# Kernel tuning notes

Measured on AMD Instinct MI355X. Metric: run time of the kernel, lower is better.

Reference implementation:

```python
import jax, jax.numpy as jnp
import numpy as np

INPUT_DIM = 256
DEPTH = 8
HIDDEN = 64
NUM_INNER = 2 ** DEPTH - 1   # 255
NUM_LEAVES = 2 ** DEPTH      # 256
BATCH = 8192


def _xavier(key, shape, fan_in, fan_out):
    bound = jnp.sqrt(6.0 / (fan_in + fan_out)).astype(jnp.float32)
    return jax.random.uniform(key, shape, jnp.float32, -bound, bound)


def setup_inputs() -> dict:
    key = jax.random.key(0)
    k = jax.random.split(key, 5)
    x = jax.random.normal(k[0], (BATCH, INPUT_DIM), jnp.float32)
    # Batched per-node MLP params (one slice per inner node)
    w1 = _xavier(k[1], (NUM_INNER, HIDDEN, INPUT_DIM), INPUT_DIM, HIDDEN)
    b1 = jnp.zeros((NUM_INNER, HIDDEN), jnp.float32)
    w2 = _xavier(k[2], (NUM_INNER, HIDDEN), HIDDEN, 1)
    b2 = jnp.zeros((NUM_INNER,), jnp.float32)
    leaf = _xavier(k[3], (NUM_LEAVES, 1), NUM_LEAVES, 1)
    return {"x": x, "w1": w1, "b1": b1, "w2": w2, "b2": b2, "leaf": leaf}


def reference(x, w1, b1, w2, b2, leaf):
    B = x.shape[0]
    # Fused per-node MLPs: hidden [B, N, H]
    h = jax.nn.relu(jnp.einsum("bi,nhi->bnh", x, w1) + b1)
    logits = jnp.einsum("bnh,nh->bn", h, w2) + b2        # [B, N]
    node_outputs = jax.nn.sigmoid(logits)                 # p, in BFS node order

    # Tree traversal: level-by-level interleave. Child of node j at a level
    # are 2j (left, weight 1-p) and 2j+1 (right, weight p) at the next level.
    reach_levels = []
    cur = jnp.ones((B, 1), x.dtype)
    for level in range(DEPTH):
        reach_levels.append(cur)
        lo = (1 << level) - 1
        p_lvl = node_outputs[:, lo : lo + (1 << level)]   # [B, 2^level]
        cur = jnp.stack([cur * (1.0 - p_lvl), cur * p_lvl], axis=-1).reshape(B, -1)
    node_reach = jnp.concatenate(reach_levels, axis=1)    # [B, NUM_INNER], BFS order
    path_probs = cur                                      # [B, NUM_LEAVES]

    h_out = (path_probs @ leaf)[:, 0]                     # [B]
    return h_out, path_probs, node_outputs, node_reach
```

## Files before the change

kernel.cpp:

```cpp
#include <hip/hip_runtime.h>
#include <cstdint>

#define BATCH   8192
#define KDIM    256
#define HID     64
#define NODES   255
#define NPG     16

typedef unsigned short u16;
typedef unsigned int u32;
typedef short bf16x8 __attribute__((ext_vector_type(8)));
typedef float f32x16 __attribute__((ext_vector_type(16)));


__device__ __forceinline__ u32 f2bf(float f) {
  u32 u = __float_as_uint(f);
  return (u + 0x7FFFu + ((u >> 16) & 1u)) >> 16;
}

__device__ __forceinline__ void gld_lds16(const void* g, void* l) {
  typedef __attribute__((address_space(1))) void* gp_t;
  typedef __attribute__((address_space(3))) void* lp_t;
  gp_t gp = reinterpret_cast<gp_t>(reinterpret_cast<uintptr_t>(g));
  lp_t lp = reinterpret_cast<lp_t>(static_cast<u32>(reinterpret_cast<uintptr_t>(l)));
  __builtin_amdgcn_global_load_lds(gp, lp, 16, 0, 0);
}


#define NPRM 16320

__global__ __launch_bounds__(256) void cvt_kernel(
    const float* __restrict__ x, const float* __restrict__ w1,
    const float* __restrict__ b1, const float* __restrict__ w2,
    u16* __restrict__ xpack, u16* __restrict__ w1pk,
    float* __restrict__ b1p, float* __restrict__ w2p) {
  const int tid = threadIdx.x;
  const int blk = blockIdx.x;

  if (blk < 256) {
    __shared__ u16 sT[32 * 268];
    const float* xs = x + (size_t)blk * 32 * KDIM;
#pragma unroll
    for (int j = 0; j < 8; ++j) {
      int idx = j * 256 + tid;
      float4 v = ((const float4*)xs)[idx];
      int row = idx >> 6, f4 = idx & 63;
      *(u32*)&sT[row * 268 + f4 * 4]     = f2bf(v.x) | (f2bf(v.y) << 16);
      *(u32*)&sT[row * 268 + f4 * 4 + 2] = f2bf(v.z) | (f2bf(v.w) << 16);
    }
    __syncthreads();
#pragma unroll
    for (int j = 0; j < 4; ++j) {
      int d = j * 256 + tid;
      int ks = d >> 6, hl = (d >> 5) & 1, l31 = d & 31;
      const u16* s8 = &sT[l31 * 268 + ks * 16 + hl * 8];
      u32 a = *(const u32*)s8, b = *(const u32*)(s8 + 2);
      u32 c = *(const u32*)(s8 + 4), e = *(const u32*)(s8 + 6);
      uint4 o = {a, b, c, e};
      ((uint4*)xpack)[(size_t)blk * 1024 + d] = o;
    }
  } else if (blk < 511) {
    __shared__ u16 sT[64 * 260];
    const int node = blk - 256;
    const float* src = w1 + (size_t)node * (HID * KDIM);
#pragma unroll
    for (int r = 0; r < 16; ++r) {
      int idx = r * 256 + tid;
      float4 v = ((const float4*)src)[idx];
      int h = idx >> 6, f4 = idx & 63;
      uint2 o;
      o.x = f2bf(v.x) | (f2bf(v.y) << 16);
      o.y = f2bf(v.z) | (f2bf(v.w) << 16);
      *(uint2*)&sT[h * 260 + f4 * 4] = o;
    }
    __syncthreads();
    u16* dst = w1pk + (size_t)node * (HID * KDIM);
#pragma unroll
    for (int r = 0; r < 8; ++r) {
      int g = r * 256 + tid;
      int kb = g >> 6, h = g & 63;
      const u16* s8 = &sT[h * 260 + kb * 8];
      uint2 lo = *(const uint2*)s8;
      uint2 hi = *(const uint2*)(s8 + 4);
      uint4 o = {lo.x, lo.y, hi.x, hi.y};
      ((uint4*)dst)[g] = o;
    }
  } else {
    int i2 = (blk - 511) * 256 + tid;
    if (i2 < 2 * NPRM) {
      int a = i2 >= NPRM;
      int j = a ? i2 - NPRM : i2;
      int reg = j & 15, rt = (j >> 4) & 1, hl = (j >> 5) & 1, node = j >> 6;
      int h = rt * 32 + (reg & 3) + 8 * (reg >> 2) + 4 * hl;
      float v = (a ? b1 : w2)[node * 64 + h];
      (a ? b1p : w2p)[j] = v;
    }
  }
}


__global__ __launch_bounds__(256, 2) void fused_mlp_kernel(
    const u16* __restrict__ xpack,
    const u16* __restrict__ w1pk,
    const float* __restrict__ b1p,
    const float* __restrict__ w2p,
    const float* __restrict__ b2,
    float* __restrict__ no_t)
{
  __shared__ __align__(16) u16 sW[2][16384];
  __shared__ __align__(16) float sW2[NPG * 64];
  __shared__ __align__(16) float sB1[NPG * 64];

  const int tid  = threadIdx.x;
  const int lane = tid & 63;
  const int wv   = tid >> 6;
  const int l31  = lane & 31;
  const int hl   = lane >> 5;
  const int nbase = blockIdx.y * NPG;

  auto stage_node = [&](int nodeIdx, int bufIdx) {
    const u16* base = w1pk + (size_t)nodeIdx * (HID * KDIM);
    char* lb = (char*)(&sW[bufIdx][0]);
#pragma unroll
    for (int j = 0; j < 8; ++j) {
      int s = j * 256 + tid;
      gld_lds16(base + s * 8, lb + s * 16);
    }
  };

  stage_node(nbase, 0);
  gld_lds16(w2p + (size_t)nbase * 64 + tid * 4, (char*)sW2 + tid * 16);
  gld_lds16(b1p + (size_t)nbase * 64 + tid * 4, (char*)sB1 + tid * 16);

  const int ctile0 = blockIdx.x * 8 + wv * 2;
  bf16x8 xf[2][16];
#pragma unroll
  for (int ct = 0; ct < 2; ++ct) {
    const u16* src = xpack + ((size_t)(ctile0 + ct) * 16) * 512 + lane * 8;
#pragma unroll
    for (int ks = 0; ks < 16; ++ks)
      xf[ct][ks] = *(const bf16x8*)(src + ks * 512);
  }

  const u32 abase = (u32)(hl * 64 + l31) * 16u;

  __syncthreads();
  int buf = 0;

  for (int i = 0; i < NPG; ++i) {
    const int node = nbase + i;

    if (i + 1 < NPG) stage_node(nbase + i + 1, buf ^ 1);

    f32x16 acc00, acc01, acc10, acc11;
    {
      const int o0 = i * 64 + hl * 32;
#pragma unroll
      for (int qd = 0; qd < 4; ++qd) {
        float4 b0 = *(const float4*)&sB1[o0 + qd * 4];
        float4 b1q = *(const float4*)&sB1[o0 + 16 + qd * 4];
#pragma unroll
        for (int e = 0; e < 4; ++e) {
          acc00[qd * 4 + e] = (&b0.x)[e];
          acc01[qd * 4 + e] = (&b0.x)[e];
          acc10[qd * 4 + e] = (&b1q.x)[e];
          acc11[qd * 4 + e] = (&b1q.x)[e];
        }
      }
    }

    const char* sw = (const char*)&sW[buf][0] + abase;
    __builtin_amdgcn_s_setprio(1);
#pragma unroll
    for (int ks = 0; ks < 16; ++ks) {
      bf16x8 a0 = *(const bf16x8*)(sw + ks * 2048);
      bf16x8 a1 = *(const bf16x8*)(sw + ks * 2048 + 512);
      acc00 = __builtin_amdgcn_mfma_f32_32x32x16_bf16(a0, xf[0][ks], acc00, 0, 0, 0);
      acc01 = __builtin_amdgcn_mfma_f32_32x32x16_bf16(a0, xf[1][ks], acc01, 0, 0, 0);
      acc10 = __builtin_amdgcn_mfma_f32_32x32x16_bf16(a1, xf[0][ks], acc10, 0, 0, 0);
      acc11 = __builtin_amdgcn_mfma_f32_32x32x16_bf16(a1, xf[1][ks], acc11, 0, 0, 0);
    }
    __builtin_amdgcn_s_setprio(0);

    float p0 = 0.f, p1 = 0.f;
#pragma unroll
    for (int qd = 0; qd < 4; ++qd) {
      int o = i * 64 + hl * 32 + qd * 4;
      float4 w0 = *(const float4*)&sW2[o];
      float4 w1q = *(const float4*)&sW2[o + 16];
#pragma unroll
      for (int e = 0; e < 4; ++e) {
        int r = qd * 4 + e;
        float w0e = (&w0.x)[e];
        float w1e = (&w1q.x)[e];
        p0 += fmaxf(acc00[r], 0.f) * w0e;
        p1 += fmaxf(acc01[r], 0.f) * w0e;
        p0 += fmaxf(acc10[r], 0.f) * w1e;
        p1 += fmaxf(acc11[r], 0.f) * w1e;
      }
    }
    p0 += __shfl_xor(p0, 32);
    p1 += __shfl_xor(p1, 32);

    if (node < NODES) {
      float pv = hl ? p1 : p0;
      float sig = 1.0f / (1.0f + expf(-(pv + b2[node])));
      no_t[(size_t)node * BATCH + blockIdx.x * 256 + wv * 64 + lane] = sig;
    }

    asm volatile("s_waitcnt vmcnt(1)" ::: "memory");
    __builtin_amdgcn_s_barrier();
    __builtin_amdgcn_sched_barrier(0);

    buf ^= 1;
  }
}


__global__ __launch_bounds__(256) void tree_kernel(
    const float* __restrict__ no_t,
    const float* __restrict__ leaf,
    float* __restrict__ out)
{
  __shared__ float p[16][257];

  const int tid = threadIdx.x;
  const int bbase = blockIdx.x * 16;
  const int wave = tid >> 6;
  const int lane = tid & 63;

  for (int i = tid; i < NODES * 16; i += 256) {
    int n = i >> 4, r = i & 15;
    p[r][n] = no_t[(size_t)n * BATCH + bbase + r];
  }
  __syncthreads();

  float4 lw = ((const float4*)leaf)[lane];

  float* h_out  = out;
  float* pp_out = out + 8192;
  float* no_out = out + 8192 + 8192 * 256;
  float* nr_out = out + 8192 + 8192 * 256 + 8192 * (size_t)NODES;

  for (int j = 0; j < 4; ++j) {
    const int r = wave * 4 + j;
    const int b = bbase + r;
    const float* pr = p[r];
    float* nr_b = nr_out + (size_t)b * NODES;

    float rc = 1.f;
#pragma unroll
    for (int L = 0; L < 6; ++L) {
      if (lane < (1 << L)) nr_b[(1 << L) - 1 + lane] = rc;
      float par = __shfl(rc, lane >> 1);
      float pv = pr[(1 << L) - 1 + (lane >> 1)];
      rc = par * ((lane & 1) ? pv : (1.f - pv));
    }
    nr_b[63 + lane] = rc;
    float p6 = pr[63 + lane];
    float r7a = rc * (1.f - p6), r7b = rc * p6;
    nr_b[127 + 2 * lane]     = r7a;
    nr_b[127 + 2 * lane + 1] = r7b;
    float p7a = pr[127 + 2 * lane], p7b = pr[127 + 2 * lane + 1];
    float4 pp;
    pp.x = r7a * (1.f - p7a);
    pp.y = r7a * p7a;
    pp.z = r7b * (1.f - p7b);
    pp.w = r7b * p7b;
    ((float4*)(pp_out + (size_t)b * 256))[lane] = pp;

    float* no_b = no_out + (size_t)b * NODES;
#pragma unroll
    for (int k = 0; k < 4; ++k) {
      int n = lane + 64 * k;
      if (n < NODES) no_b[n] = pr[n];
    }

    float hacc = pp.x * lw.x + pp.y * lw.y + pp.z * lw.z + pp.w * lw.w;
    hacc += __shfl_xor(hacc, 1);
    hacc += __shfl_xor(hacc, 2);
    hacc += __shfl_xor(hacc, 4);
    hacc += __shfl_xor(hacc, 8);
    hacc += __shfl_xor(hacc, 16);
    hacc += __shfl_xor(hacc, 32);
    if (lane == 0) h_out[b] = hacc;
  }
}


extern "C" void kernel_launch(void* const* d_in, const int* in_sizes, int n_in,
                              void* d_out, int out_size, void* d_ws, size_t ws_size,
                              hipStream_t stream) {
  const float* x    = (const float*)d_in[0];
  const float* w1   = (const float*)d_in[1];
  const float* b1   = (const float*)d_in[2];
  const float* w2   = (const float*)d_in[3];
  const float* b2   = (const float*)d_in[4];
  const float* leaf = (const float*)d_in[5];
  float* out = (float*)d_out;

  char* ws = (char*)d_ws;
  u16*   xpack = (u16*)ws;
  u16*   w1pk  = (u16*)(ws + (size_t)4194304);
  float* w2p   = (float*)(ws + (size_t)12582912);
  float* b1p   = (float*)(ws + (size_t)12648192);
  float* no_t  = (float*)(ws + (size_t)12713472);

  cvt_kernel<<<639, 256, 0, stream>>>(x, w1, b1, w2, xpack, w1pk, b1p, w2p);

  dim3 g(32, 16);
  fused_mlp_kernel<<<g, 256, 0, stream>>>(xpack, w1pk, b1p, w2p, b2, no_t);

  tree_kernel<<<BATCH / 16, 256, 0, stream>>>(no_t, leaf, out);
}
```

Before: 153.9 us.

## Split K into halves, stream x from global, and shrink node groups for occupancy

Nodes per block drop from 16 to 4, so the grid grows to 32x64 blocks. W1 staging is split into two K-halves in a 2x8192 LDS buffer. Only half of the x fragments stay in registers, and the other half is reloaded from global memory between the two half-MFMA passes. The goal is to cut registers and LDS so that three blocks fit per CU, and to spread work over more blocks. In exchange, x is re-read from global/L2 for every node, and each node now needs extra barriers.

```diff
diff --git a/kernel.cpp b/kernel.cpp
--- a/kernel.cpp
+++ b/kernel.cpp
@@ -5,7 +5,7 @@
 #define KDIM    256
 #define HID     64
 #define NODES   255
-#define NPG     16
+#define NPG     4
 
 typedef unsigned short u16;
 typedef unsigned int u32;
@@ -99,7 +99,7 @@
 }
 
 
-__global__ __launch_bounds__(256, 2) void fused_mlp_kernel(
+__global__ __launch_bounds__(256, 3) void fused_mlp_kernel(
     const u16* __restrict__ xpack,
     const u16* __restrict__ w1pk,
     const float* __restrict__ b1p,
@@ -107,7 +107,7 @@
     const float* __restrict__ b2,
     float* __restrict__ no_t)
 {
-  __shared__ __align__(16) u16 sW[2][16384];
+  __shared__ __align__(16) u16 sW[2][8192];
   __shared__ __align__(16) float sW2[NPG * 64];
   __shared__ __align__(16) float sB1[NPG * 64];
 
@@ -118,46 +118,50 @@
   const int hl   = lane >> 5;
   const int nbase = blockIdx.y * NPG;
 
-  auto stage_node = [&](int nodeIdx, int bufIdx) {
-    const u16* base = w1pk + (size_t)nodeIdx * (HID * KDIM);
+  auto stage_half = [&](int iLocal, int half, int bufIdx) {
+    const u16* base = w1pk + (size_t)(nbase + iLocal) * 16384 + half * 8192;
     char* lb = (char*)(&sW[bufIdx][0]);
 #pragma unroll
-    for (int j = 0; j < 8; ++j) {
+    for (int j = 0; j < 4; ++j) {
       int s = j * 256 + tid;
       gld_lds16(base + s * 8, lb + s * 16);
     }
   };
 
-  stage_node(nbase, 0);
-  gld_lds16(w2p + (size_t)nbase * 64 + tid * 4, (char*)sW2 + tid * 16);
-  gld_lds16(b1p + (size_t)nbase * 64 + tid * 4, (char*)sB1 + tid * 16);
+  stage_half(0, 0, 0);
+  if (tid < 64) {
+    gld_lds16(w2p + (size_t)nbase * 64 + tid * 4, (char*)sW2 + tid * 16);
+  } else if (tid < 128) {
+    int t = tid - 64;
+    gld_lds16(b1p + (size_t)nbase * 64 + t * 4, (char*)sB1 + t * 16);
+  }
 
   const int ctile0 = blockIdx.x * 8 + wv * 2;
-  bf16x8 xf[2][16];
-#pragma unroll
-  for (int ct = 0; ct < 2; ++ct) {
-    const u16* src = xpack + ((size_t)(ctile0 + ct) * 16) * 512 + lane * 8;
-#pragma unroll
-    for (int ks = 0; ks < 16; ++ks)
-      xf[ct][ks] = *(const bf16x8*)(src + ks * 512);
+  const u16* xs0 = xpack + (size_t)(ctile0 + 0) * 8192 + lane * 8;
+  const u16* xs1 = xpack + (size_t)(ctile0 + 1) * 8192 + lane * 8;
+  bf16x8 xf0[8], xf1[8];
+#pragma unroll
+  for (int ks = 0; ks < 8; ++ks) {
+    xf0[ks] = *(const bf16x8*)(xs0 + ks * 512);
+    xf1[ks] = *(const bf16x8*)(xs1 + ks * 512);
   }
 
   const u32 abase = (u32)(hl * 64 + l31) * 16u;
 
   __syncthreads();
-  int buf = 0;
 
   for (int i = 0; i < NPG; ++i) {
-    const int node = nbase + i;
-
-    if (i + 1 < NPG) stage_node(nbase + i + 1, buf ^ 1);
+    const int fc = i & 1;
+    const int oc = fc ^ 1;
+
+    stage_half(i, oc, 1);
 
     f32x16 acc00, acc01, acc10, acc11;
     {
       const int o0 = i * 64 + hl * 32;
 #pragma unroll
       for (int qd = 0; qd < 4; ++qd) {
-        float4 b0 = *(const float4*)&sB1[o0 + qd * 4];
+        float4 b0  = *(const float4*)&sB1[o0 + qd * 4];
         float4 b1q = *(const float4*)&sB1[o0 + 16 + qd * 4];
 #pragma unroll
         for (int e = 0; e < 4; ++e) {
@@ -169,50 +173,65 @@
       }
     }
 
-    const char* sw = (const char*)&sW[buf][0] + abase;
-    __builtin_amdgcn_s_setprio(1);
-#pragma unroll
-    for (int ks = 0; ks < 16; ++ks) {
-      bf16x8 a0 = *(const bf16x8*)(sw + ks * 2048);
-      bf16x8 a1 = *(const bf16x8*)(sw + ks * 2048 + 512);
-      acc00 = __builtin_amdgcn_mfma_f32_32x32x16_bf16(a0, xf[0][ks], acc00, 0, 0, 0);
-      acc01 = __builtin_amdgcn_mfma_f32_32x32x16_bf16(a0, xf[1][ks], acc01, 0, 0, 0);
-      acc10 = __builtin_amdgcn_mfma_f32_32x32x16_bf16(a1, xf[0][ks], acc10, 0, 0, 0);
-      acc11 = __builtin_amdgcn_mfma_f32_32x32x16_bf16(a1, xf[1][ks], acc11, 0, 0, 0);
-    }
-    __builtin_amdgcn_s_setprio(0);
+    {
+      const char* sw = (const char*)&sW[0][0] + abase;
+      const u16* nx0 = xs0 + oc * 4096;
+      const u16* nx1 = xs1 + oc * 4096;
+#pragma unroll
+      for (int ks = 0; ks < 8; ++ks) {
+        bf16x8 a0 = *(const bf16x8*)(sw + ks * 2048);
+        bf16x8 a1 = *(const bf16x8*)(sw + ks * 2048 + 512);
+        acc00 = __builtin_amdgcn_mfma_f32_32x32x16_bf16(a0, xf0[ks], acc00, 0, 0, 0);
+        acc01 = __builtin_amdgcn_mfma_f32_32x32x16_bf16(a0, xf1[ks], acc01, 0, 0, 0);
+        acc10 = __builtin_amdgcn_mfma_f32_32x32x16_bf16(a1, xf0[ks], acc10, 0, 0, 0);
+        acc11 = __builtin_amdgcn_mfma_f32_32x32x16_bf16(a1, xf1[ks], acc11, 0, 0, 0);
+        xf0[ks] = *(const bf16x8*)(nx0 + ks * 512);
+        xf1[ks] = *(const bf16x8*)(nx1 + ks * 512);
+      }
+    }
+    __syncthreads();
+
+    if (i + 1 < NPG) stage_half(i + 1, oc, 0);
+
+    {
+      const char* sw = (const char*)&sW[1][0] + abase;
+#pragma unroll
+      for (int ks = 0; ks < 8; ++ks) {
+        bf16x8 a0 = *(const bf16x8*)(sw + ks * 2048);
+        bf16x8 a1 = *(const bf16x8*)(sw + ks * 2048 + 512);
+        acc00 = __builtin_amdgcn_mfma_f32_32x32x16_bf16(a0, xf0[ks], acc00, 0, 0, 0);
+        acc01 = __builtin_amdgcn_mfma_f32_32x32x16_bf16(a0, xf1[ks], acc01, 0, 0, 0);
+        acc10 = __builtin_amdgcn_mfma_f32_32x32x16_bf16(a1, xf0[ks], acc10, 0, 0, 0);
+        acc11 = __builtin_amdgcn_mfma_f32_32x32x16_bf16(a1, xf1[ks], acc11, 0, 0, 0);
+      }
+    }
 
     float p0 = 0.f, p1 = 0.f;
 #pragma unroll
     for (int qd = 0; qd < 4; ++qd) {
       int o = i * 64 + hl * 32 + qd * 4;
-      float4 w0 = *(const float4*)&sW2[o];
+      float4 w0  = *(const float4*)&sW2[o];
       float4 w1q = *(const float4*)&sW2[o + 16];
 #pragma unroll
       for (int e = 0; e < 4; ++e) {
         int r = qd * 4 + e;
-        float w0e = (&w0.x)[e];
-        float w1e = (&w1q.x)[e];
-        p0 += fmaxf(acc00[r], 0.f) * w0e;
-        p1 += fmaxf(acc01[r], 0.f) * w0e;
-        p0 += fmaxf(acc10[r], 0.f) * w1e;
-        p1 += fmaxf(acc11[r], 0.f) * w1e;
+        p0 += fmaxf(acc00[r], 0.f) * (&w0.x)[e];
+        p1 += fmaxf(acc01[r], 0.f) * (&w0.x)[e];
+        p0 += fmaxf(acc10[r], 0.f) * (&w1q.x)[e];
+        p1 += fmaxf(acc11[r], 0.f) * (&w1q.x)[e];
       }
     }
     p0 += __shfl_xor(p0, 32);
     p1 += __shfl_xor(p1, 32);
 
+    const int node = nbase + i;
     if (node < NODES) {
       float pv = hl ? p1 : p0;
       float sig = 1.0f / (1.0f + expf(-(pv + b2[node])));
       no_t[(size_t)node * BATCH + blockIdx.x * 256 + wv * 64 + lane] = sig;
     }
 
-    asm volatile("s_waitcnt vmcnt(1)" ::: "memory");
-    __builtin_amdgcn_s_barrier();
-    __builtin_amdgcn_sched_barrier(0);
-
-    buf ^= 1;
+    if (i + 1 < NPG) __syncthreads();
   }
 }
 
@@ -308,7 +327,7 @@
 
   cvt_kernel<<<639, 256, 0, stream>>>(x, w1, b1, w2, xpack, w1pk, b1p, w2p);
 
-  dim3 g(32, 16);
+  dim3 g(32, 64);
   fused_mlp_kernel<<<g, 256, 0, stream>>>(xpack, w1pk, b1p, w2p, b2, no_t);
 
   tree_kernel<<<BATCH / 16, 256, 0, stream>>>(no_t, leaf, out);
```

Result: slower. 162.2 us (+5.4%).

## Merge three kernels into one cooperative persistent kernel with grid syncs

Applied to the files above, without the earlier changes.

Replaces the separate convert, fused-MLP and tree kernels with a single cooperative launch that loops over the old block indices and uses grid-wide syncs between phases. Shared memory is a union so each phase reuses the same allocation. The aim is to remove the launch gaps and tail effects between kernels. In exchange it adds grid.sync overhead and hipOccupancy queries on the host. It also replaces the per-node vmcnt-based wait with a full __syncthreads, which may weaken the overlap between staging and MFMA.

```diff
diff --git a/kernel.cpp b/kernel.cpp
--- a/kernel.cpp
+++ b/kernel.cpp
@@ -1,11 +1,15 @@
 #include <hip/hip_runtime.h>
+#include <hip/hip_cooperative_groups.h>
 #include <cstdint>
+
+namespace cg = cooperative_groups;
 
 #define BATCH   8192
 #define KDIM    256
 #define HID     64
 #define NODES   255
 #define NPG     16
+#define NPRM    16320
 
 typedef unsigned short u16;
 typedef unsigned int u32;
@@ -27,263 +31,256 @@
 }
 
 
-#define NPRM 16320
-
-__global__ __launch_bounds__(256) void cvt_kernel(
+__global__ __launch_bounds__(256, 2) void mega_kernel(
     const float* __restrict__ x, const float* __restrict__ w1,
     const float* __restrict__ b1, const float* __restrict__ w2,
+    const float* __restrict__ b2, const float* __restrict__ leaf,
     u16* __restrict__ xpack, u16* __restrict__ w1pk,
-    float* __restrict__ b1p, float* __restrict__ w2p) {
-  const int tid = threadIdx.x;
-  const int blk = blockIdx.x;
-
-  if (blk < 256) {
-    __shared__ u16 sT[32 * 268];
-    const float* xs = x + (size_t)blk * 32 * KDIM;
-#pragma unroll
-    for (int j = 0; j < 8; ++j) {
-      int idx = j * 256 + tid;
-      float4 v = ((const float4*)xs)[idx];
-      int row = idx >> 6, f4 = idx & 63;
-      *(u32*)&sT[row * 268 + f4 * 4]     = f2bf(v.x) | (f2bf(v.y) << 16);
-      *(u32*)&sT[row * 268 + f4 * 4 + 2] = f2bf(v.z) | (f2bf(v.w) << 16);
-    }
-    __syncthreads();
-#pragma unroll
-    for (int j = 0; j < 4; ++j) {
-      int d = j * 256 + tid;
-      int ks = d >> 6, hl = (d >> 5) & 1, l31 = d & 31;
-      const u16* s8 = &sT[l31 * 268 + ks * 16 + hl * 8];
-      u32 a = *(const u32*)s8, b = *(const u32*)(s8 + 2);
-      u32 c = *(const u32*)(s8 + 4), e = *(const u32*)(s8 + 6);
-      uint4 o = {a, b, c, e};
-      ((uint4*)xpack)[(size_t)blk * 1024 + d] = o;
-    }
-  } else if (blk < 511) {
-    __shared__ u16 sT[64 * 260];
-    const int node = blk - 256;
-    const float* src = w1 + (size_t)node * (HID * KDIM);
-#pragma unroll
-    for (int r = 0; r < 16; ++r) {
-      int idx = r * 256 + tid;
-      float4 v = ((const float4*)src)[idx];
-      int h = idx >> 6, f4 = idx & 63;
-      uint2 o;
-      o.x = f2bf(v.x) | (f2bf(v.y) << 16);
-      o.y = f2bf(v.z) | (f2bf(v.w) << 16);
-      *(uint2*)&sT[h * 260 + f4 * 4] = o;
-    }
-    __syncthreads();
-    u16* dst = w1pk + (size_t)node * (HID * KDIM);
-#pragma unroll
-    for (int r = 0; r < 8; ++r) {
-      int g = r * 256 + tid;
-      int kb = g >> 6, h = g & 63;
-      const u16* s8 = &sT[h * 260 + kb * 8];
-      uint2 lo = *(const uint2*)s8;
-      uint2 hi = *(const uint2*)(s8 + 4);
-      uint4 o = {lo.x, lo.y, hi.x, hi.y};
-      ((uint4*)dst)[g] = o;
-    }
-  } else {
-    int i2 = (blk - 511) * 256 + tid;
-    if (i2 < 2 * NPRM) {
-      int a = i2 >= NPRM;
-      int j = a ? i2 - NPRM : i2;
-      int reg = j & 15, rt = (j >> 4) & 1, hl = (j >> 5) & 1, node = j >> 6;
-      int h = rt * 32 + (reg & 3) + 8 * (reg >> 2) + 4 * hl;
-      float v = (a ? b1 : w2)[node * 64 + h];
-      (a ? b1p : w2p)[j] = v;
-    }
-  }
-}
-
-
-__global__ __launch_bounds__(256, 2) void fused_mlp_kernel(
-    const u16* __restrict__ xpack,
-    const u16* __restrict__ w1pk,
-    const float* __restrict__ b1p,
-    const float* __restrict__ w2p,
-    const float* __restrict__ b2,
-    float* __restrict__ no_t)
+    float* __restrict__ b1p, float* __restrict__ w2p,
+    float* __restrict__ no_t, float* __restrict__ out)
 {
-  __shared__ __align__(16) u16 sW[2][16384];
-  __shared__ __align__(16) float sW2[NPG * 64];
-  __shared__ __align__(16) float sB1[NPG * 64];
+  cg::grid_group grid = cg::this_grid();
+
+  __shared__ __align__(16) union ShU {
+    struct { u16 sW[2][16384]; float sW2[NPG * 64]; float sB1[NPG * 64]; } f;
+    u16 cx[32 * 268];
+    u16 cw[64 * 260];
+    float tp[16][257];
+  } sh;
 
   const int tid  = threadIdx.x;
   const int lane = tid & 63;
   const int wv   = tid >> 6;
   const int l31  = lane & 31;
   const int hl   = lane >> 5;
-  const int nbase = blockIdx.y * NPG;
-
-  auto stage_node = [&](int nodeIdx, int bufIdx) {
-    const u16* base = w1pk + (size_t)nodeIdx * (HID * KDIM);
-    char* lb = (char*)(&sW[bufIdx][0]);
-#pragma unroll
-    for (int j = 0; j < 8; ++j) {
-      int s = j * 256 + tid;
-      gld_lds16(base + s * 8, lb + s * 16);
-    }
-  };
-
-  stage_node(nbase, 0);
-  gld_lds16(w2p + (size_t)nbase * 64 + tid * 4, (char*)sW2 + tid * 16);
-  gld_lds16(b1p + (size_t)nbase * 64 + tid * 4, (char*)sB1 + tid * 16);
-
-  const int ctile0 = blockIdx.x * 8 + wv * 2;
-  bf16x8 xf[2][16];
-#pragma unroll
-  for (int ct = 0; ct < 2; ++ct) {
-    const u16* src = xpack + ((size_t)(ctile0 + ct) * 16) * 512 + lane * 8;
-#pragma unroll
-    for (int ks = 0; ks < 16; ++ks)
-      xf[ct][ks] = *(const bf16x8*)(src + ks * 512);
+
+  for (int blk = blockIdx.x; blk < 639; blk += gridDim.x) {
+    if (blk < 256) {
+      u16* sT = sh.cx;
+      const float* xs = x + (size_t)blk * 32 * KDIM;
+#pragma unroll
+      for (int j = 0; j < 8; ++j) {
+        int idx = j * 256 + tid;
+        float4 v = ((const float4*)xs)[idx];
+        int row = idx >> 6, f4 = idx & 63;
+        *(u32*)&sT[row * 268 + f4 * 4]     = f2bf(v.x) | (f2bf(v.y) << 16);
+        *(u32*)&sT[row * 268 + f4 * 4 + 2] = f2bf(v.z) | (f2bf(v.w) << 16);
+      }
+      __syncthreads();
+#pragma unroll
+      for (int j = 0; j < 4; ++j) {
+        int d = j * 256 + tid;
+        int ks = d >> 6, hh = (d >> 5) & 1, ll = d & 31;
+        const u16* s8 = &sT[ll * 268 + ks * 16 + hh * 8];
+        u32 a = *(const u32*)s8, b = *(const u32*)(s8 + 2);
+        u32 c = *(const u32*)(s8 + 4), e = *(const u32*)(s8 + 6);
+        uint4 o = {a, b, c, e};
+        ((uint4*)xpack)[(size_t)blk * 1024 + d] = o;
+      }
+    } else if (blk < 511) {
+      u16* sT = sh.cw;
+      const int node = blk - 256;
+      const float* src = w1 + (size_t)node * (HID * KDIM);
+#pragma unroll
+      for (int r = 0; r < 16; ++r) {
+        int idx = r * 256 + tid;
+        float4 v = ((const float4*)src)[idx];
+        int h = idx >> 6, f4 = idx & 63;
+        uint2 o;
+        o.x = f2bf(v.x) | (f2bf(v.y) << 16);
+        o.y = f2bf(v.z) | (f2bf(v.w) << 16);
+        *(uint2*)&sT[h * 260 + f4 * 4] = o;
+      }
+      __syncthreads();
+      u16* dst = w1pk + (size_t)node * (HID * KDIM);
+#pragma unroll
+      for (int r = 0; r < 8; ++r) {
+        int g = r * 256 + tid;
+        int kb = g >> 6, h = g & 63;
+        const u16* s8 = &sT[h * 260 + kb * 8];
+        uint2 lo = *(const uint2*)s8;
+        uint2 hi = *(const uint2*)(s8 + 4);
+        uint4 o = {lo.x, lo.y, hi.x, hi.y};
+        ((uint4*)dst)[g] = o;
+      }
+    } else {
+      int i2 = (blk - 511) * 256 + tid;
+      if (i2 < 2 * NPRM) {
+        int a = i2 >= NPRM;
+        int j = a ? i2 - NPRM : i2;
+        int reg = j & 15, rt = (j >> 4) & 1, hh = (j >> 5) & 1, node = j >> 6;
+        int h = rt * 32 + (reg & 3) + 8 * (reg >> 2) + 4 * hh;
+        float v = (a ? b1 : w2)[node * 64 + h];
+        (a ? b1p : w2p)[j] = v;
+      }
+    }
+    __syncthreads();
   }
 
-  const u32 abase = (u32)(hl * 64 + l31) * 16u;
-
-  __syncthreads();
-  int buf = 0;
-
-  for (int i = 0; i < NPG; ++i) {
-    const int node = nbase + i;
-
-    if (i + 1 < NPG) stage_node(nbase + i + 1, buf ^ 1);
-
-    f32x16 acc00, acc01, acc10, acc11;
-    {
-      const int o0 = i * 64 + hl * 32;
+  __threadfence();
+  grid.sync();
+
+  for (int fb = blockIdx.x; fb < 512; fb += gridDim.x) {
+    const int bx = fb & 31;
+    const int by = fb >> 5;
+    const int nbase = by * NPG;
+
+    auto stage_node = [&](int nodeIdx, int bufIdx) {
+      const u16* base = w1pk + (size_t)nodeIdx * (HID * KDIM);
+      char* lb = (char*)(&sh.f.sW[bufIdx][0]);
+#pragma unroll
+      for (int j = 0; j < 8; ++j) {
+        int s = j * 256 + tid;
+        gld_lds16(base + s * 8, lb + s * 16);
+      }
+    };
+
+    stage_node(nbase, 0);
+    gld_lds16(w2p + (size_t)nbase * 64 + tid * 4, (char*)sh.f.sW2 + tid * 16);
+    gld_lds16(b1p + (size_t)nbase * 64 + tid * 4, (char*)sh.f.sB1 + tid * 16);
+
+    const int ctile0 = bx * 8 + wv * 2;
+    bf16x8 xf[2][16];
+#pragma unroll
+    for (int ct = 0; ct < 2; ++ct) {
+      const u16* src = xpack + ((size_t)(ctile0 + ct) * 16) * 512 + lane * 8;
+#pragma unroll
+      for (int ks = 0; ks < 16; ++ks)
+        xf[ct][ks] = *(const bf16x8*)(src + ks * 512);
+    }
+
+    const u32 abase = (u32)(hl * 64 + l31) * 16u;
+
+    __syncthreads();
+    int buf = 0;
+
+    for (int i = 0; i < NPG; ++i) {
+      const int node = nbase + i;
+
+      if (i + 1 < NPG) stage_node(nbase + i + 1, buf ^ 1);
+
+      f32x16 acc00, acc01, acc10, acc11;
+      {
+        const int o0 = i * 64 + hl * 32;
+#pragma unroll
+        for (int qd = 0; qd < 4; ++qd) {
+          float4 b0  = *(const float4*)&sh.f.sB1[o0 + qd * 4];
+          float4 b1q = *(const float4*)&sh.f.sB1[o0 + 16 + qd * 4];
+#pragma unroll
+          for (int e = 0; e < 4; ++e) {
+            acc00[qd * 4 + e] = (&b0.x)[e];
+            acc01[qd * 4 + e] = (&b0.x)[e];
+            acc10[qd * 4 + e] = (&b1q.x)[e];
+            acc11[qd * 4 + e] = (&b1q.x)[e];
+          }
+        }
+      }
+
+      const char* sw = (const char*)&sh.f.sW[buf][0] + abase;
+      __builtin_amdgcn_s_setprio(1);
+#pragma unroll
+      for (int ks = 0; ks < 16; ++ks) {
+        bf16x8 a0 = *(const bf16x8*)(sw + ks * 2048);
+        bf16x8 a1 = *(const bf16x8*)(sw + ks * 2048 + 512);
+        acc00 = __builtin_amdgcn_mfma_f32_32x32x16_bf16(a0, xf[0][ks], acc00, 0, 0, 0);
+        acc01 = __builtin_amdgcn_mfma_f32_32x32x16_bf16(a0, xf[1][ks], acc01, 0, 0, 0);
+        acc10 = __builtin_amdgcn_mfma_f32_32x32x16_bf16(a1, xf[0][ks], acc10, 0, 0, 0);
+        acc11 = __builtin_amdgcn_mfma_f32_32x32x16_bf16(a1, xf[1][ks], acc11, 0, 0, 0);
+      }
+      __builtin_amdgcn_s_setprio(0);
+
+      float p0 = 0.f, p1 = 0.f;
 #pragma unroll
       for (int qd = 0; qd < 4; ++qd) {
-        float4 b0 = *(const float4*)&sB1[o0 + qd * 4];
-        float4 b1q = *(const float4*)&sB1[o0 + 16 + qd * 4];
+        int o = i * 64 + hl * 32 + qd * 4;
+        float4 w0  = *(const float4*)&sh.f.sW2[o];
+        float4 w1q = *(const float4*)&sh.f.sW2[o + 16];
 #pragma unroll
         for (int e = 0; e < 4; ++e) {
-          acc00[qd * 4 + e] = (&b0.x)[e];
-          acc01[qd * 4 + e] = (&b0.x)[e];
-          acc10[qd * 4 + e] = (&b1q.x)[e];
-          acc11[qd * 4 + e] = (&b1q.x)[e];
+          int r = qd * 4 + e;
+          p0 += fmaxf(acc00[r], 0.f) * (&w0.x)[e];
+          p1 += fmaxf(acc01[r], 0.f) * (&w0.x)[e];
+          p0 += fmaxf(acc10[r], 0.f) * (&w1q.x)[e];
+          p1 += fmaxf(acc11[r], 0.f) * (&w1q.x)[e];
         }
       }
-    }
-
-    const char* sw = (const char*)&sW[buf][0] + abase;
-    __builtin_amdgcn_s_setprio(1);
-#pragma unroll
-    for (int ks = 0; ks < 16; ++ks) {
-      bf16x8 a0 = *(const bf16x8*)(sw + ks * 2048);
-      bf16x8 a1 = *(const bf16x8*)(sw + ks * 2048 + 512);
-      acc00 = __builtin_amdgcn_mfma_f32_32x32x16_bf16(a0, xf[0][ks], acc00, 0, 0, 0);
-      acc01 = __builtin_amdgcn_mfma_f32_32x32x16_bf16(a0, xf[1][ks], acc01, 0, 0, 0);
-      acc10 = __builtin_amdgcn_mfma_f32_32x32x16_bf16(a1, xf[0][ks], acc10, 0, 0, 0);
-      acc11 = __builtin_amdgcn_mfma_f32_32x32x16_bf16(a1, xf[1][ks], acc11, 0, 0, 0);
-    }
-    __builtin_amdgcn_s_setprio(0);
-
-    float p0 = 0.f, p1 = 0.f;
-#pragma unroll
-    for (int qd = 0; qd < 4; ++qd) {
-      int o = i * 64 + hl * 32 + qd * 4;
-      float4 w0 = *(const float4*)&sW2[o];
-      float4 w1q = *(const float4*)&sW2[o + 16];
-#pragma unroll
-      for (int e = 0; e < 4; ++e) {
-        int r = qd * 4 + e;
-        float w0e = (&w0.x)[e];
-        float w1e = (&w1q.x)[e];
-        p0 += fmaxf(acc00[r], 0.f) * w0e;
-        p1 += fmaxf(acc01[r], 0.f) * w0e;
-        p0 += fmaxf(acc10[r], 0.f) * w1e;
-        p1 += fmaxf(acc11[r], 0.f) * w1e;
-      }
-    }
-    p0 += __shfl_xor(p0, 32);
-    p1 += __shfl_xor(p1, 32);
-
-    if (node < NODES) {
-      float pv = hl ? p1 : p0;
-      float sig = 1.0f / (1.0f + expf(-(pv + b2[node])));
-      no_t[(size_t)node * BATCH + blockIdx.x * 256 + wv * 64 + lane] = sig;
-    }
-
-    asm volatile("s_waitcnt vmcnt(1)" ::: "memory");
-    __builtin_amdgcn_s_barrier();
-    __builtin_amdgcn_sched_barrier(0);
-
-    buf ^= 1;
+      p0 += __shfl_xor(p0, 32);
+      p1 += __shfl_xor(p1, 32);
+
+      if (node < NODES) {
+        float pv = hl ? p1 : p0;
+        float sig = 1.0f / (1.0f + expf(-(pv + b2[node])));
+        no_t[(size_t)node * BATCH + bx * 256 + wv * 64 + lane] = sig;
+      }
+
+      __syncthreads();
+      buf ^= 1;
+    }
   }
-}
-
-
-__global__ __launch_bounds__(256) void tree_kernel(
-    const float* __restrict__ no_t,
-    const float* __restrict__ leaf,
-    float* __restrict__ out)
-{
-  __shared__ float p[16][257];
-
-  const int tid = threadIdx.x;
-  const int bbase = blockIdx.x * 16;
-  const int wave = tid >> 6;
-  const int lane = tid & 63;
-
-  for (int i = tid; i < NODES * 16; i += 256) {
-    int n = i >> 4, r = i & 15;
-    p[r][n] = no_t[(size_t)n * BATCH + bbase + r];
-  }
-  __syncthreads();
-
-  float4 lw = ((const float4*)leaf)[lane];
-
-  float* h_out  = out;
-  float* pp_out = out + 8192;
-  float* no_out = out + 8192 + 8192 * 256;
-  float* nr_out = out + 8192 + 8192 * 256 + 8192 * (size_t)NODES;
-
-  for (int j = 0; j < 4; ++j) {
-    const int r = wave * 4 + j;
-    const int b = bbase + r;
-    const float* pr = p[r];
-    float* nr_b = nr_out + (size_t)b * NODES;
-
-    float rc = 1.f;
-#pragma unroll
-    for (int L = 0; L < 6; ++L) {
-      if (lane < (1 << L)) nr_b[(1 << L) - 1 + lane] = rc;
-      float par = __shfl(rc, lane >> 1);
-      float pv = pr[(1 << L) - 1 + (lane >> 1)];
-      rc = par * ((lane & 1) ? pv : (1.f - pv));
-    }
-    nr_b[63 + lane] = rc;
-    float p6 = pr[63 + lane];
-    float r7a = rc * (1.f - p6), r7b = rc * p6;
-    nr_b[127 + 2 * lane]     = r7a;
-    nr_b[127 + 2 * lane + 1] = r7b;
-    float p7a = pr[127 + 2 * lane], p7b = pr[127 + 2 * lane + 1];
-    float4 pp;
-    pp.x = r7a * (1.f - p7a);
-    pp.y = r7a * p7a;
-    pp.z = r7b * (1.f - p7b);
-    pp.w = r7b * p7b;
-    ((float4*)(pp_out + (size_t)b * 256))[lane] = pp;
-
-    float* no_b = no_out + (size_t)b * NODES;
-#pragma unroll
-    for (int k = 0; k < 4; ++k) {
-      int n = lane + 64 * k;
-      if (n < NODES) no_b[n] = pr[n];
-    }
-
-    float hacc = pp.x * lw.x + pp.y * lw.y + pp.z * lw.z + pp.w * lw.w;
-    hacc += __shfl_xor(hacc, 1);
-    hacc += __shfl_xor(hacc, 2);
-    hacc += __shfl_xor(hacc, 4);
-    hacc += __shfl_xor(hacc, 8);
-    hacc += __shfl_xor(hacc, 16);
-    hacc += __shfl_xor(hacc, 32);
-    if (lane == 0) h_out[b] = hacc;
+
+  __threadfence();
+  grid.sync();
+
+  for (int tb = blockIdx.x; tb < 512; tb += gridDim.x) {
+    const int bbase = tb * 16;
+
+    for (int i = tid; i < NODES * 16; i += 256) {
+      int n = i >> 4, r = i & 15;
+      sh.tp[r][n] = no_t[(size_t)n * BATCH + bbase + r];
+    }
+    __syncthreads();
+
+    float4 lw = ((const float4*)leaf)[lane];
+
+    float* h_out  = out;
+    float* pp_out = out + 8192;
+    float* no_out = out + 8192 + 8192 * 256;
+    float* nr_out = out + 8192 + 8192 * 256 + 8192 * (size_t)NODES;
+
+    for (int j = 0; j < 4; ++j) {
+      const int r = wv * 4 + j;
+      const int b = bbase + r;
+      const float* pr = sh.tp[r];
+      float* nr_b = nr_out + (size_t)b * NODES;
+
+      float rc = 1.f;
+#pragma unroll
+      for (int L = 0; L < 6; ++L) {
+        if (lane < (1 << L)) nr_b[(1 << L) - 1 + lane] = rc;
+        float par = __shfl(rc, lane >> 1);
+        float pv = pr[(1 << L) - 1 + (lane >> 1)];
+        rc = par * ((lane & 1) ? pv : (1.f - pv));
+      }
+      nr_b[63 + lane] = rc;
+      float p6 = pr[63 + lane];
+      float r7a = rc * (1.f - p6), r7b = rc * p6;
+      nr_b[127 + 2 * lane]     = r7a;
+      nr_b[127 + 2 * lane + 1] = r7b;
+      float p7a = pr[127 + 2 * lane], p7b = pr[127 + 2 * lane + 1];
+      float4 pp;
+      pp.x = r7a * (1.f - p7a);
+      pp.y = r7a * p7a;
+      pp.z = r7b * (1.f - p7b);
+      pp.w = r7b * p7b;
+      ((float4*)(pp_out + (size_t)b * 256))[lane] = pp;
+
+      float* no_b = no_out + (size_t)b * NODES;
+#pragma unroll
+      for (int k = 0; k < 4; ++k) {
+        int n = lane + 64 * k;
+        if (n < NODES) no_b[n] = pr[n];
+      }
+
+      float hacc = pp.x * lw.x + pp.y * lw.y + pp.z * lw.z + pp.w * lw.w;
+      hacc += __shfl_xor(hacc, 1);
+      hacc += __shfl_xor(hacc, 2);
+      hacc += __shfl_xor(hacc, 4);
+      hacc += __shfl_xor(hacc, 8);
+      hacc += __shfl_xor(hacc, 16);
+      hacc += __shfl_xor(hacc, 32);
+      if (lane == 0) h_out[b] = hacc;
+    }
+    __syncthreads();
   }
 }
 
@@ -306,10 +303,18 @@
   float* b1p   = (float*)(ws + (size_t)12648192);
   float* no_t  = (float*)(ws + (size_t)12713472);
 
-  cvt_kernel<<<639, 256, 0, stream>>>(x, w1, b1, w2, xpack, w1pk, b1p, w2p);
-
-  dim3 g(32, 16);
-  fused_mlp_kernel<<<g, 256, 0, stream>>>(xpack, w1pk, b1p, w2p, b2, no_t);
-
-  tree_kernel<<<BATCH / 16, 256, 0, stream>>>(no_t, leaf, out);
+  int maxBlk = 0;
+  (void)hipOccupancyMaxActiveBlocksPerMultiprocessor(
+      &maxBlk, reinterpret_cast<const void*>(mega_kernel), 256, 0);
+  int grid = maxBlk * 256;
+  if (grid > 512) grid = 512;
+  if (grid < 256) grid = 256;
+
+  void* args[12] = {
+    (void*)&x, (void*)&w1, (void*)&b1, (void*)&w2, (void*)&b2, (void*)&leaf,
+    (void*)&xpack, (void*)&w1pk, (void*)&b1p, (void*)&w2p, (void*)&no_t,
+    (void*)&out
+  };
+  hipLaunchCooperativeKernel(reinterpret_cast<const void*>(mega_kernel),
+                             dim3(grid), dim3(256), args, 0, stream);
 }
```

After: 299.1 us. 1.94x slower.
